# Performance work log

Measured on AMD Instinct MI355X. Metric: run time of the kernel, lower is better.

## Reference

```python
import jax, jax.numpy as jnp
import numpy as np

B, N, D = 32, 2048, 768
DEPTH, HEADS, GRID, NC = 12, 12, 10, 40
T = GRID * GRID + 1          # 100 pillars + cls token
HD = D // HEADS
SCALE = HD ** -0.5
INTERVAL = 0.2
MLP_H = 4 * D
EPS = 1e-5


def setup_inputs() -> dict:
    key = jax.random.key(0)
    ks = list(jax.random.split(key, 12))
    n = lambda k, s, std: (jax.random.normal(k, s, dtype=jnp.float32) * std)
    return {
        "x": jax.random.uniform(ks[0], (B, N, 3), minval=-1.0, maxval=1.0, dtype=jnp.float32),
        "W1": n(ks[1], (6, 32), 0.1),
        "W2": n(ks[2], (32, 64), 0.1),
        "W3": n(ks[3], (64, 128), 0.1),
        "Wa": n(ks[4], (256, D), 0.05),
        "bn_g": jnp.ones((GRID * GRID,), jnp.float32),
        "bn_b": jnp.zeros((GRID * GRID,), jnp.float32),
        "bn_mean": jnp.zeros((GRID * GRID,), jnp.float32),
        "bn_var": jnp.ones((GRID * GRID,), jnp.float32),
        "cls_token": jnp.zeros((1, 1, D), jnp.float32),
        "pos_embed": n(ks[5], (1, T, D), 0.02),
        "ln1_g": jnp.ones((DEPTH, D), jnp.float32), "ln1_b": jnp.zeros((DEPTH, D), jnp.float32),
        "qkv_w": n(ks[6], (DEPTH, D, 3 * D), 0.01),
        "proj_w": n(ks[7], (DEPTH, D, D), 0.01), "proj_b": jnp.zeros((DEPTH, D), jnp.float32),
        "ln2_g": jnp.ones((DEPTH, D), jnp.float32), "ln2_b": jnp.zeros((DEPTH, D), jnp.float32),
        "fc1_w": n(ks[8], (DEPTH, D, MLP_H), 0.01), "fc1_b": jnp.zeros((DEPTH, MLP_H), jnp.float32),
        "fc2_w": n(ks[9], (DEPTH, MLP_H, D), 0.01), "fc2_b": jnp.zeros((DEPTH, D), jnp.float32),
        "norm_g": jnp.ones((D,), jnp.float32), "norm_b": jnp.zeros((D,), jnp.float32),
        "head_w": n(ks[10], (D, NC), 0.01), "head_b": jnp.zeros((NC,), jnp.float32),
    }


def _layer_norm(x, g, b):
    m = jnp.mean(x, -1, keepdims=True)
    v = jnp.mean(jnp.square(x - m), -1, keepdims=True)
    return (x - m) * jax.lax.rsqrt(v + EPS) * g + b


def reference(x, W1, W2, W3, Wa, bn_g, bn_b, bn_mean, bn_var, cls_token, pos_embed,
              ln1_g, ln1_b, qkv_w, proj_w, proj_b, ln2_g, ln2_b,
              fc1_w, fc1_b, fc2_w, fc2_b, norm_g, norm_b, head_w, head_b):
    # ---- Pillar encoder (voxel bucketing via segment ops) ----
    # torch code reorders columns (y,z,x)->(z,y,x); voxel index uses (y,x)
    p = x[..., jnp.array([1, 0, 2])]                     # [B,N,3] = (z,y,x)
    yx = jnp.clip(p[..., 1:] + 1.0, 0.0, 1.99)
    idx = jnp.floor(yx / INTERVAL).astype(jnp.int32)     # [B,N,2] in [0,GRID)
    cell = (idx[..., 0] * GRID + idx[..., 1]
            + jnp.arange(B, dtype=jnp.int32)[:, None] * GRID * GRID).reshape(-1)
    pf = p.reshape(-1, 3)                                # [B*N,3]
    S = B * GRID * GRID
    cnt = jax.ops.segment_sum(jnp.ones((B * N,), pf.dtype), cell, num_segments=S)
    centroid = jax.ops.segment_sum(pf, cell, num_segments=S) / jnp.maximum(cnt, 1.0)[:, None]
    aug = jnp.concatenate([pf, pf - centroid[cell]], -1)  # [B*N,6]
    h = jax.nn.relu(aug @ W1)
    h = jax.nn.relu(h @ W2)
    h = jax.nn.relu(h @ W3)                               # [B*N,128]
    pooled = jax.ops.segment_max(h, cell, num_segments=S)  # per-pillar max
    h2 = jax.nn.relu(jnp.concatenate([h, pooled[cell]], -1) @ Wa)  # [B*N,768]
    pillar = jax.ops.segment_max(h2, cell, num_segments=S)
    pillar = jnp.where(cnt[:, None] > 0, pillar, 0.0)     # empty cells stay zero
    seq = pillar.reshape(B, GRID * GRID, D)               # flatten order = y*GRID+x
    # BatchNorm1d(100) over the sequence-position channel (eval mode)
    inv = bn_g * jax.lax.rsqrt(bn_var + EPS)
    seq = (seq - bn_mean[None, :, None]) * inv[None, :, None] + bn_b[None, :, None]

    # ---- ViT stack ----
    tokens = jnp.concatenate([jnp.broadcast_to(cls_token, (B, 1, D)), seq], 1) + pos_embed

    def block(hh, prm):
        g1, b1, qw, pw, pb, g2, b2, f1w, f1b, f2w, f2b = prm
        y = _layer_norm(hh, g1, b1)
        qkv = (y @ qw).reshape(B, T, 3, HEADS, HD)
        q, k, v = qkv[:, :, 0], qkv[:, :, 1], qkv[:, :, 2]   # [B,T,H,hd]
        attn = jax.nn.softmax(jnp.einsum('bqhd,bkhd->bhqk', q, k) * SCALE, -1)
        o = jnp.einsum('bhqk,bkhd->bqhd', attn, v).reshape(B, T, D)
        hh = hh + o @ pw + pb
        y = _layer_norm(hh, g2, b2)
        y = jax.nn.gelu(y @ f1w + f1b, approximate=False)
        hh = hh + y @ f2w + f2b
        return hh, None

    prms = (ln1_g, ln1_b, qkv_w, proj_w, proj_b, ln2_g, ln2_b, fc1_w, fc1_b, fc2_w, fc2_b)
    tokens, _ = jax.lax.scan(block, tokens, prms)
    out = _layer_norm(tokens, norm_g, norm_b)[:, 0] @ head_w + head_b  # cls head
    return out
```

## Files before the change

kernel.cpp:

```cpp
#include <hip/hip_runtime.h>

typedef __bf16 bf8 __attribute__((ext_vector_type(8)));
typedef float  f4  __attribute__((ext_vector_type(4)));
typedef unsigned long long uptr;

__device__ __forceinline__ void gload16(const void* g, void* l){
  __builtin_amdgcn_global_load_lds(
      (const __attribute__((address_space(1))) unsigned int*)(uptr)g,
      (__attribute__((address_space(3))) unsigned int*)(uptr)l,
      16, 0, 0);
}

__device__ __forceinline__ int xcd_chunk(int d, int nwg){
  int q = nwg >> 3, r = nwg & 7;
  int c = d & 7, j = d >> 3;
  return c*q + (c < r ? c : r) + j;
}


__global__ __launch_bounds__(256) void k_cell(const float* __restrict__ x, int* __restrict__ cellArr,
                                              float* __restrict__ cnt, float* __restrict__ cent){
  int p = blockIdx.x*256 + threadIdx.x;
  float x0 = x[p*3+0], x1 = x[p*3+1], x2 = x[p*3+2];
  float y0 = fminf(fmaxf(x0 + 1.0f, 0.0f), 1.99f);
  float y1 = fminf(fmaxf(x2 + 1.0f, 0.0f), 1.99f);
  int i0 = (int)floorf(y0 / 0.2f);
  int i1 = (int)floorf(y1 / 0.2f);
  int b = p >> 11;
  int cell = b*100 + i0*10 + i1;
  cellArr[p] = cell;
  atomicAdd(&cnt[cell], 1.0f);
  atomicAdd(&cent[cell*3+0], x1);
  atomicAdd(&cent[cell*3+1], x0);
  atomicAdd(&cent[cell*3+2], x2);
}

__global__ __launch_bounds__(256) void k_scan(const float* __restrict__ cnt,
                                              int* __restrict__ base, int* __restrict__ wptr){
  __shared__ int a[256];
  int tid = threadIdx.x;
  int start = tid*13, end = start+13; if (end > 3200) end = 3200;
  int local = 0;
  for (int i = start; i < end; i++) local += (int)cnt[i];
  a[tid] = local;
  __syncthreads();
  for (int off = 1; off < 256; off <<= 1){
    int t = (tid >= off) ? a[tid - off] : 0;
    __syncthreads();
    a[tid] += t;
    __syncthreads();
  }
  int run = a[tid] - local;
  for (int i = start; i < end; i++){
    base[i] = run; wptr[i] = run;
    run += (int)cnt[i];
  }
}

__global__ __launch_bounds__(256) void k_scatter(const int* __restrict__ cellArr,
                                                 int* __restrict__ wptr, int* __restrict__ order){
  int p = blockIdx.x*256 + threadIdx.x;
  int c = cellArr[p];
  int pos = atomicAdd(&wptr[c], 1);
  order[pos] = p;
}

__global__ __launch_bounds__(256) void k_pointmlp(const float* __restrict__ x,
    const float* __restrict__ W1, const float* __restrict__ W2, const float* __restrict__ W3,
    const float* __restrict__ cent, const float* __restrict__ cnt, const int* __restrict__ cellArr,
    const int* __restrict__ order, int* __restrict__ cellSlot, __bf16* __restrict__ A2){
  __shared__ float w1s[6*32];
  __shared__ float w2s[32*64];
  __shared__ float w3s[64*128];
  int tid = threadIdx.x;
  for (int i = tid; i < 192;  i += 256) w1s[i] = W1[i];
  for (int i = tid; i < 2048; i += 256) w2s[i] = W2[i];
  for (int i = tid; i < 8192; i += 256) w3s[i] = W3[i];
  __syncthreads();
  int s = blockIdx.x*256 + tid;
  int p = order[s];
  int cell = cellArr[p];
  cellSlot[s] = cell;
  float pf0 = x[p*3+1], pf1 = x[p*3+0], pf2 = x[p*3+2];
  float cc = fmaxf(cnt[cell], 1.0f);
  float a[6] = {pf0, pf1, pf2,
                pf0 - cent[cell*3+0]/cc, pf1 - cent[cell*3+1]/cc, pf2 - cent[cell*3+2]/cc};
  float h1[32];
  #pragma unroll
  for (int f = 0; f < 32; f++){
    float t = 0.f;
    #pragma unroll
    for (int i = 0; i < 6; i++) t += a[i]*w1s[i*32+f];
    h1[f] = fmaxf(t, 0.f);
  }
  float h2[64];
  #pragma unroll
  for (int f = 0; f < 64; f++){
    float t = 0.f;
    #pragma unroll
    for (int i = 0; i < 32; i++) t += h1[i]*w2s[i*64+f];
    h2[f] = fmaxf(t, 0.f);
  }
  for (int f0 = 0; f0 < 128; f0 += 8){
    __bf16 tmp[8];
    #pragma unroll
    for (int j = 0; j < 8; j++){
      float t = 0.f;
      #pragma unroll
      for (int i = 0; i < 64; i++) t += h2[i]*w3s[i*128+f0+j];
      tmp[j] = (__bf16)fmaxf(t, 0.f);
    }
    *reinterpret_cast<uint4*>(&A2[(size_t)s*256 + f0]) = *reinterpret_cast<uint4*>(tmp);
  }
}

__global__ __launch_bounds__(128) void k_poolh(const __bf16* __restrict__ A2,
    const int* __restrict__ base, const float* __restrict__ cnt, float* __restrict__ pooled){
  int c = blockIdx.x, f = threadIdx.x;
  int b0 = base[c], n = (int)cnt[c];
  float v = 0.f;
  for (int k = 0; k < n; k++) v = fmaxf(v, (float)A2[(size_t)(b0+k)*256 + f]);
  pooled[c*128 + f] = v;
}

__global__ __launch_bounds__(256) void k_fill(const float* __restrict__ pooled,
    const int* __restrict__ cellSlot, __bf16* __restrict__ A2){
  int idx = blockIdx.x*256 + threadIdx.x;
  int s = idx >> 4, f0 = (idx & 15) << 3;
  int cell = cellSlot[s];
  const float* pp = &pooled[cell*128 + f0];
  __bf16 tmp[8];
  #pragma unroll
  for (int j = 0; j < 8; j++) tmp[j] = (__bf16)pp[j];
  *reinterpret_cast<uint4*>(&A2[(size_t)s*256 + 128 + f0]) = *reinterpret_cast<uint4*>(tmp);
}

__global__ __launch_bounds__(256) void k_pillarpool(const __bf16* __restrict__ h2c,
    const int* __restrict__ base, const float* __restrict__ cnt, float* __restrict__ pillar){
  int c = blockIdx.x, tid = threadIdx.x;
  int b0 = base[c], n = (int)cnt[c];
  if (n == 0) return;
  for (int f = tid; f < 768; f += 256){
    float v = 0.f;
    for (int s = b0; s < b0 + n; s++) v = fmaxf(v, (float)h2c[(size_t)s*768 + f]);
    pillar[(size_t)c*768 + f] = v;
  }
}

__global__ void k_assemble(const float* __restrict__ pillar,
    const float* __restrict__ bn_g, const float* __restrict__ bn_b,
    const float* __restrict__ bn_mean, const float* __restrict__ bn_var,
    const float* __restrict__ cls_t, const float* __restrict__ pos,
    float* __restrict__ tokens){
  int idx = blockIdx.x*256 + threadIdx.x;
  int m = idx / 768, d = idx % 768;
  int b = m / 101, t = m % 101;
  float v;
  if (t == 0) v = cls_t[d];
  else {
    int s = t - 1;
    float pv = pillar[((size_t)b*100 + s)*768 + d];
    float inv = bn_g[s]*rsqrtf(bn_var[s] + 1e-5f);
    v = (pv - bn_mean[s])*inv + bn_b[s];
  }
  tokens[idx] = v + pos[t*768 + d];
}

__global__ __launch_bounds__(256) void k_transpose_all(
    const float* __restrict__ qw, const float* __restrict__ pw,
    const float* __restrict__ f1, const float* __restrict__ f2,
    const float* __restrict__ wa,
    __bf16* __restrict__ wq, __bf16* __restrict__ wp,
    __bf16* __restrict__ w1, __bf16* __restrict__ w2,
    __bf16* __restrict__ wwa){
  int id = blockIdx.x;
  size_t l = blockIdx.y;
  const float* W; __bf16* Wt; int K, N, kx, nx;
  if (id >= 1728){
    if (l != 0) return;
    id -= 1728; W=wa; Wt=wwa; K=256; N=768; kx=id%2; nx=id/2;
  }
  else if (id < 432){          W=qw+l*768*2304; Wt=wq+l*768*2304; K=768;  N=2304; kx=id%6;  nx=id/6; }
  else if (id < 576){ id-=432; W=pw+l*768*768;  Wt=wp+l*768*768;  K=768;  N=768;  kx=id%6;  nx=id/6; }
  else if (id < 1152){ id-=576;  W=f1+l*768*3072; Wt=w1+l*768*3072; K=768;  N=3072; kx=id%6;  nx=id/6; }
  else {               id-=1152; W=f2+l*3072*768; Wt=w2+l*3072*768; K=3072; N=768;  kx=id%24; nx=id/24; }
  __shared__ __bf16 t[32*136];
  int k0 = kx*128, n0 = nx*32;
  int tid = threadIdx.x;
  int kr = tid >> 3, nc = (tid & 7)*4;
  #pragma unroll
  for (int i = 0; i < 4; i++){
    int k = kr + i*32;
    float4 v = *reinterpret_cast<const float4*>(&W[(size_t)(k0+k)*N + n0 + nc]);
    float vv[4] = {v.x, v.y, v.z, v.w};
    #pragma unroll
    for (int jj = 0; jj < 4; jj++){
      int n = nc + jj;
      int slot = (k >> 3) ^ ((n >> 1) & 7);
      t[n*136 + slot*8 + (k & 7)] = (__bf16)vv[jj];
    }
  }
  __syncthreads();
  int nr = tid >> 4, sl = tid & 15;
  #pragma unroll
  for (int j = 0; j < 2; j++){
    int n = j*16 + nr;
    int slot = sl ^ ((n >> 1) & 7);
    *reinterpret_cast<uint4*>(&Wt[(size_t)(n0+n)*K + k0 + sl*8]) =
        *reinterpret_cast<uint4*>(&t[n*136 + slot*8]);
  }
}


__global__ __launch_bounds__(256) void k_gemm(const __bf16* __restrict__ A, const __bf16* __restrict__ Bt,
    const float* __restrict__ bias, const float* __restrict__ res,
    float* __restrict__ outF, __bf16* __restrict__ outB,
    int M, int N, int K, int act, int splitK){
  __shared__ alignas(16) __bf16 As[128*64];
  __shared__ alignas(16) __bf16 Bs[128*64];
  int tid  = threadIdx.x;
  int gx = gridDim.x, gy = gridDim.y;
  int d = blockIdx.y*gx + blockIdx.x;
  int w = xcd_chunk(d, gx*gy);
  int nx = w / gy, my = w % gy;
  int m0 = my*128, n0 = nx*128;
  int z = blockIdx.z;
  int kLen = K / splitK, k0 = z*kLen;
  int wave = tid >> 6, lane = tid & 63;
  int wm = (wave >> 1)*64, wn = (wave & 1)*64;
  int r16 = lane & 15, q = lane >> 4;
  int srow = tid >> 3;
  int sslot = tid & 7;
  int slotX[2];
  #pragma unroll
  for (int kk = 0; kk < 2; kk++) slotX[kk] = ((kk*4 + q) ^ (r16 & 7)) * 8;
  f4 acc[4][4];
  #pragma unroll
  for (int i = 0; i < 4; i++)
    #pragma unroll
    for (int j = 0; j < 4; j++) acc[i][j] = (f4){0.f,0.f,0.f,0.f};

  for (int kt = k0; kt < k0 + kLen; kt += 64){
    #pragma unroll
    for (int rr = 0; rr < 4; rr++){
      int row = rr*32 + srow;
      int scol = kt + ((sslot ^ (row & 7)) * 8);
      int gm = m0 + row; if (gm >= M) gm = M - 1;
      gload16(A  + (size_t)gm*K + scol, (char*)As + rr*4096 + tid*16);
      int gn = n0 + row;
      gload16(Bt + (size_t)gn*K + scol, (char*)Bs + rr*4096 + tid*16);
    }
    __syncthreads();
    #pragma unroll
    for (int kk = 0; kk < 2; kk++){
      bf8 af[4], bq[4];
      #pragma unroll
      for (int i = 0; i < 4; i++) af[i] = *reinterpret_cast<const bf8*>(&As[(wm + i*16 + r16)*64 + slotX[kk]]);
      #pragma unroll
      for (int j = 0; j < 4; j++) bq[j] = *reinterpret_cast<const bf8*>(&Bs[(wn + j*16 + r16)*64 + slotX[kk]]);
      #pragma unroll
      for (int i = 0; i < 4; i++)
        #pragma unroll
        for (int j = 0; j < 4; j++)
          acc[i][j] = __builtin_amdgcn_mfma_f32_16x16x32_bf16(af[i], bq[j], acc[i][j], 0, 0, 0);
    }
    __syncthreads();
  }

  #pragma unroll
  for (int i = 0; i < 4; i++){
    #pragma unroll
    for (int j = 0; j < 4; j++){
      int nn = n0 + wn + j*16 + r16;
      float bv = (bias && z == 0) ? bias[nn] : 0.f;
      #pragma unroll
      for (int r = 0; r < 4; r++){
        int m = m0 + wm + i*16 + q*4 + r;
        if (m >= M) continue;
        float v = acc[i][j][r] + bv;
        if (splitK > 1){
          atomicAdd(&outF[(size_t)m*N + nn], v);
        } else {
          if (act == 1) v = fmaxf(v, 0.f);
          else if (act == 2) v = 0.5f*v*(1.f + erff(v*0.70710678118654752f));
          if (outB){
            outB[(size_t)m*N + nn] = (__bf16)v;
          } else {
            float rv = res ? res[(size_t)m*N + nn] : 0.f;
            outF[(size_t)m*N + nn] = rv + v;
          }
        }
      }
    }
  }
}


__global__ __launch_bounds__(256) void k_ln(const float* __restrict__ in, const float* __restrict__ g,
    const float* __restrict__ bta, __bf16* __restrict__ outB, float* __restrict__ outF, int rowMul){
  int orow = blockIdx.x;
  const float* xr = in + (size_t)orow*rowMul*768;
  int tid = threadIdx.x;
  float v0 = xr[tid], v1 = xr[tid+256], v2 = xr[tid+512];
  float s = v0+v1+v2, s2 = v0*v0 + v1*v1 + v2*v2;
  #pragma unroll
  for (int off = 32; off > 0; off >>= 1){ s += __shfl_xor(s, off); s2 += __shfl_xor(s2, off); }
  __shared__ float rs[4], rq[4];
  int w = tid >> 6;
  if ((tid & 63) == 0){ rs[w] = s; rq[w] = s2; }
  __syncthreads();
  s = rs[0]+rs[1]+rs[2]+rs[3]; s2 = rq[0]+rq[1]+rq[2]+rq[3];
  float mean = s*(1.f/768.f);
  float var  = s2*(1.f/768.f) - mean*mean;
  float rstd = rsqrtf(var + 1e-5f);
  size_t ob = (size_t)orow*768;
  float y0 = (v0-mean)*rstd*g[tid]     + bta[tid];
  float y1 = (v1-mean)*rstd*g[tid+256] + bta[tid+256];
  float y2 = (v2-mean)*rstd*g[tid+512] + bta[tid+512];
  if (outB){ outB[ob+tid]=(__bf16)y0; outB[ob+tid+256]=(__bf16)y1; outB[ob+tid+512]=(__bf16)y2; }
  else     { outF[ob+tid]=y0;         outF[ob+tid+256]=y1;         outF[ob+tid+512]=y2; }
}


#define PSS 136
#define VTS 136

__global__ __launch_bounds__(256, 3) void k_attn(const __bf16* __restrict__ qkvB, __bf16* __restrict__ o){
  __shared__ alignas(16) __bf16 smem[64*VTS + 64*PSS];
  __bf16* Vt = smem;
  __bf16* Ps = smem + 64*VTS;
  int w = xcd_chunk(blockIdx.x, gridDim.x);
  int bh = w >> 1, half = w & 1;
  int b = bh / 12, h = bh % 12;
  int tid = threadIdx.x;
  const __bf16* basep = qkvB + (size_t)(b*101)*2304 + h*64;

  #pragma unroll
  for (int it = 0; it < 4; it++){
    int c = tid + it*256;
    int t = c >> 3, d0 = c & 7;
    bf8 v;
    if (t < 101){
      v = *reinterpret_cast<const bf8*>(&basep[(size_t)t*2304 + 1536 + d0*8]);
    } else {
      #pragma unroll
      for (int j = 0; j < 8; j++) v[j] = (__bf16)0.f;
    }
    #pragma unroll
    for (int j = 0; j < 8; j++){
      int jj = (j + d0) & 7;
      Vt[(d0*8 + jj)*VTS + t] = v[jj];
    }
  }

  int wave = tid >> 6, lane = tid & 63;
  int r16 = lane & 15, q = lane >> 4;
  int m0 = half*64 + wave*16;

  f4 sacc[7];
  #pragma unroll
  for (int j = 0; j < 7; j++) sacc[j] = (f4){0.f,0.f,0.f,0.f};
  #pragma unroll
  for (int kt = 0; kt < 64; kt += 32){
    int row = m0 + r16; if (row > 100) row = 100;
    bf8 aq = *reinterpret_cast<const bf8*>(&basep[(size_t)row*2304 + kt + q*8]);
    #pragma unroll
    for (int j = 0; j < 7; j++){
      int krow = j*16 + r16; if (krow > 100) krow = 100;
      bf8 kf = *reinterpret_cast<const bf8*>(&basep[(size_t)krow*2304 + 768 + kt + q*8]);
      sacc[j] = __builtin_amdgcn_mfma_f32_16x16x32_bf16(aq, kf, sacc[j], 0, 0, 0);
    }
  }

  #pragma unroll
  for (int r = 0; r < 4; r++){
    float s[7];
    #pragma unroll
    for (int j = 0; j < 7; j++){
      s[j] = sacc[j][r] * 0.125f;
      if (j == 6 && r16 >= 5) s[j] = -1e30f;
    }
    float mx = s[0];
    #pragma unroll
    for (int j = 1; j < 7; j++) mx = fmaxf(mx, s[j]);
    #pragma unroll
    for (int off2 = 1; off2 < 16; off2 <<= 1) mx = fmaxf(mx, __shfl_xor(mx, off2));
    float p[7], sum = 0.f;
    #pragma unroll
    for (int j = 0; j < 7; j++){ p[j] = __expf(s[j] - mx); sum += p[j]; }
    #pragma unroll
    for (int off2 = 1; off2 < 16; off2 <<= 1) sum += __shfl_xor(sum, off2);
    float inv = 1.f / sum;
    int lr = wave*16 + q*4 + r;
    #pragma unroll
    for (int j = 0; j < 7; j++) Ps[lr*PSS + j*16 + r16] = (__bf16)(p[j]*inv);
    Ps[lr*PSS + 112 + r16] = (__bf16)0.f;
  }
  __syncthreads();

  f4 oacc[4];
  #pragma unroll
  for (int n = 0; n < 4; n++) oacc[n] = (f4){0.f,0.f,0.f,0.f};
  #pragma unroll
  for (int kt = 0; kt < 128; kt += 32){
    bf8 af = *reinterpret_cast<const bf8*>(&Ps[(wave*16 + r16)*PSS + kt + q*8]);
    #pragma unroll
    for (int n = 0; n < 4; n++){
      bf8 bq = *reinterpret_cast<const bf8*>(&Vt[(n*16 + r16)*VTS + kt + q*8]);
      oacc[n] = __builtin_amdgcn_mfma_f32_16x16x32_bf16(af, bq, oacc[n], 0, 0, 0);
    }
  }

  #pragma unroll
  for (int n = 0; n < 4; n++){
    #pragma unroll
    for (int r = 0; r < 4; r++){
      int t = m0 + q*4 + r;
      if (t < 101)
        o[((size_t)(b*101 + t))*768 + h*64 + n*16 + r16] = (__bf16)oacc[n][r];
    }
  }
}

__global__ __launch_bounds__(256) void k_head(const float* __restrict__ cls, const float* __restrict__ hw,
                       const float* __restrict__ hb, float* __restrict__ out){
  int b = blockIdx.x;
  int tid = threadIdx.x;
  int c = tid % 40, s = tid / 40;
  __shared__ float part[6][40];
  if (s < 6){
    float acc = 0.f;
    for (int k = s*128; k < s*128 + 128; k++) acc += cls[b*768 + k]*hw[k*40 + c];
    part[s][c] = acc;
  }
  __syncthreads();
  if (tid < 40){
    float v = hb[tid];
    #pragma unroll
    for (int i = 0; i < 6; i++) v += part[i][tid];
    out[b*40 + tid] = v;
  }
}


extern "C" void kernel_launch(void* const* d_in, const int* in_sizes, int n_in,
                              void* d_out, int out_size, void* d_ws, size_t ws_size,
                              hipStream_t stream){
  const float* x       = (const float*)d_in[0];
  const float* W1      = (const float*)d_in[1];
  const float* W2      = (const float*)d_in[2];
  const float* W3      = (const float*)d_in[3];
  const float* Wa      = (const float*)d_in[4];
  const float* bn_g    = (const float*)d_in[5];
  const float* bn_b    = (const float*)d_in[6];
  const float* bn_mean = (const float*)d_in[7];
  const float* bn_var  = (const float*)d_in[8];
  const float* cls_t   = (const float*)d_in[9];
  const float* pos     = (const float*)d_in[10];
  const float* ln1_g   = (const float*)d_in[11];
  const float* ln1_b   = (const float*)d_in[12];
  const float* qkv_w   = (const float*)d_in[13];
  const float* proj_w  = (const float*)d_in[14];
  const float* proj_b  = (const float*)d_in[15];
  const float* ln2_g   = (const float*)d_in[16];
  const float* ln2_b   = (const float*)d_in[17];
  const float* fc1_w   = (const float*)d_in[18];
  const float* fc1_b   = (const float*)d_in[19];
  const float* fc2_w   = (const float*)d_in[20];
  const float* fc2_b   = (const float*)d_in[21];
  const float* norm_g  = (const float*)d_in[22];
  const float* norm_b  = (const float*)d_in[23];
  const float* head_w  = (const float*)d_in[24];
  const float* head_b  = (const float*)d_in[25];

  char* ws = (char*)d_ws;
  size_t off = 0;
  auto alloc = [&](size_t bytes)->void*{ void* p = ws + off; off += (bytes + 255) & ~(size_t)255; return p; };
  float* cnt     = (float*)alloc(3200*4);
  float* cent    = (float*)alloc(3200*3*4);
  float* pillar  = (float*)alloc((size_t)3200*768*4);
  size_t zbytes  = (size_t)((char*)pillar - (char*)cnt) + (size_t)3200*768*4;
  int*   base    = (int*)  alloc(3200*4);
  int*   wptr    = (int*)  alloc(3200*4);
  int*   order   = (int*)  alloc((size_t)65536*4);
  int*   cellSlot= (int*)  alloc((size_t)65536*4);
  int*   cellArr = (int*)  alloc((size_t)65536*4);
  float* pooled  = (float*)alloc((size_t)3200*128*4);
  float* tokens  = (float*)alloc((size_t)3232*768*4);
  float* cls     = (float*)alloc((size_t)32*768*4);
  __bf16* wWa    = (__bf16*)alloc((size_t)768*256*2);
  __bf16* wq12   = (__bf16*)alloc((size_t)12*768*2304*2);
  __bf16* wp12   = (__bf16*)alloc((size_t)12*768*768*2);
  __bf16* w112   = (__bf16*)alloc((size_t)12*768*3072*2);
  __bf16* w212   = (__bf16*)alloc((size_t)12*3072*768*2);
  size_t offR = off;
  __bf16* A2  = (__bf16*)alloc((size_t)65536*256*2);
  __bf16* h2c = (__bf16*)alloc((size_t)65536*768*2);
  size_t endPillarPhase = off;
  off = offR;
  __bf16* y    = (__bf16*)alloc((size_t)3232*768*2);
  __bf16* qkvB = (__bf16*)alloc((size_t)3232*2304*2);
  __bf16* o    = (__bf16*)alloc((size_t)3232*768*2);
  __bf16* mlp  = (__bf16*)alloc((size_t)3232*3072*2);
  if (off < endPillarPhase) off = endPillarPhase;
  (void)ws_size; (void)in_sizes; (void)n_in; (void)out_size;

  hipMemsetAsync(cnt, 0, zbytes, stream);

  k_transpose_all<<<dim3(1776,12),256,0,stream>>>(qkv_w, proj_w, fc1_w, fc2_w, Wa,
                                                  wq12, wp12, w112, w212, wWa);

  k_cell<<<256,256,0,stream>>>(x, cellArr, cnt, cent);
  k_scan<<<1,256,0,stream>>>(cnt, base, wptr);
  k_scatter<<<256,256,0,stream>>>(cellArr, wptr, order);
  k_pointmlp<<<256,256,0,stream>>>(x, W1, W2, W3, cent, cnt, cellArr, order, cellSlot, A2);
  k_poolh<<<3200,128,0,stream>>>(A2, base, cnt, pooled);
  k_fill<<<4096,256,0,stream>>>(pooled, cellSlot, A2);
  k_gemm<<<dim3(6,512),256,0,stream>>>(A2, wWa, nullptr, nullptr, nullptr, h2c, 65536, 768, 256, 1, 1);
  k_pillarpool<<<3200,256,0,stream>>>(h2c, base, cnt, pillar);
  k_assemble<<<9696,256,0,stream>>>(pillar, bn_g, bn_b, bn_mean, bn_var, cls_t, pos, tokens);

  for (int l = 0; l < 12; l++){
    __bf16* wq = wq12 + (size_t)l*768*2304;
    __bf16* wp = wp12 + (size_t)l*768*768;
    __bf16* w1 = w112 + (size_t)l*768*3072;
    __bf16* w2 = w212 + (size_t)l*3072*768;
    k_ln<<<3232,256,0,stream>>>(tokens, ln1_g + l*768, ln1_b + l*768, y, nullptr, 1);
    k_gemm<<<dim3(18,26),256,0,stream>>>(y, wq, nullptr, nullptr, nullptr, qkvB, 3232, 2304, 768, 0, 1);
    k_attn<<<768,256,0,stream>>>(qkvB, o);
    k_gemm<<<dim3(6,26,4),256,0,stream>>>(o, wp, proj_b + l*768, nullptr, tokens, nullptr,
                                          3232, 768, 768, 0, 4);
    k_ln<<<3232,256,0,stream>>>(tokens, ln2_g + l*768, ln2_b + l*768, y, nullptr, 1);
    k_gemm<<<dim3(24,26),256,0,stream>>>(y, w1, fc1_b + l*3072, nullptr, nullptr, mlp, 3232, 3072, 768, 2, 1);
    k_gemm<<<dim3(6,26,4),256,0,stream>>>(mlp, w2, fc2_b + l*768, nullptr, tokens, nullptr,
                                          3232, 768, 3072, 0, 4);
  }

  k_ln<<<32,256,0,stream>>>(tokens, norm_g, norm_b, nullptr, cls, 101);
  k_head<<<32,256,0,stream>>>(cls, head_w, head_b, (float*)d_out);
}
```

Before: 2.830 ms.

## Fuse pillar max-pool into Wa GEMM, vectorize LN and assemble, halve split-K

The Wa GEMM now max-reduces its ReLU outputs straight into the per-cell pillar buffer with integer atomicMax. This removes the 65536x768 bf16 intermediate and the separate pillar pool kernel. LayerNorm now processes one row per wave with float4 loads and no shared-memory reduction, and the token assembly kernel is vectorized with float4. Split-K for the proj and fc2 GEMMs drops from 4 to 2, cutting atomic traffic but giving fewer workgroups. The atomicMax-on-int trick relies on nonnegative values and a zeroed buffer, and it adds atomic contention on the pillar rows.

```diff
diff --git a/kernel.cpp b/kernel.cpp
--- a/kernel.cpp
+++ b/kernel.cpp
@@ -135,35 +135,30 @@
   *reinterpret_cast<uint4*>(&A2[(size_t)s*256 + 128 + f0]) = *reinterpret_cast<uint4*>(tmp);
 }
 
-__global__ __launch_bounds__(256) void k_pillarpool(const __bf16* __restrict__ h2c,
-    const int* __restrict__ base, const float* __restrict__ cnt, float* __restrict__ pillar){
-  int c = blockIdx.x, tid = threadIdx.x;
-  int b0 = base[c], n = (int)cnt[c];
-  if (n == 0) return;
-  for (int f = tid; f < 768; f += 256){
-    float v = 0.f;
-    for (int s = b0; s < b0 + n; s++) v = fmaxf(v, (float)h2c[(size_t)s*768 + f]);
-    pillar[(size_t)c*768 + f] = v;
-  }
-}
-
-__global__ void k_assemble(const float* __restrict__ pillar,
+__global__ __launch_bounds__(256) void k_assemble(const float* __restrict__ pillar,
     const float* __restrict__ bn_g, const float* __restrict__ bn_b,
     const float* __restrict__ bn_mean, const float* __restrict__ bn_var,
     const float* __restrict__ cls_t, const float* __restrict__ pos,
     float* __restrict__ tokens){
   int idx = blockIdx.x*256 + threadIdx.x;
-  int m = idx / 768, d = idx % 768;
+  int m = idx / 192, d4 = (idx % 192)*4;
   int b = m / 101, t = m % 101;
-  float v;
-  if (t == 0) v = cls_t[d];
-  else {
+  float4 pv = *reinterpret_cast<const float4*>(&pos[t*768 + d4]);
+  float4 out;
+  if (t == 0){
+    float4 ct = *reinterpret_cast<const float4*>(&cls_t[d4]);
+    out.x = ct.x + pv.x; out.y = ct.y + pv.y; out.z = ct.z + pv.z; out.w = ct.w + pv.w;
+  } else {
     int s = t - 1;
-    float pv = pillar[((size_t)b*100 + s)*768 + d];
+    float4 p = *reinterpret_cast<const float4*>(&pillar[((size_t)b*100 + s)*768 + d4]);
     float inv = bn_g[s]*rsqrtf(bn_var[s] + 1e-5f);
-    v = (pv - bn_mean[s])*inv + bn_b[s];
-  }
-  tokens[idx] = v + pos[t*768 + d];
+    float mu = bn_mean[s], bb = bn_b[s];
+    out.x = (p.x - mu)*inv + bb + pv.x;
+    out.y = (p.y - mu)*inv + bb + pv.y;
+    out.z = (p.z - mu)*inv + bb + pv.z;
+    out.w = (p.w - mu)*inv + bb + pv.w;
+  }
+  *reinterpret_cast<float4*>(&tokens[(size_t)m*768 + d4]) = out;
 }
 
 __global__ __launch_bounds__(256) void k_transpose_all(
@@ -215,7 +210,7 @@
 __global__ __launch_bounds__(256) void k_gemm(const __bf16* __restrict__ A, const __bf16* __restrict__ Bt,
     const float* __restrict__ bias, const float* __restrict__ res,
     float* __restrict__ outF, __bf16* __restrict__ outB,
-    int M, int N, int K, int act, int splitK){
+    int M, int N, int K, int act, int splitK, const int* __restrict__ cellSlot){
   __shared__ alignas(16) __bf16 As[128*64];
   __shared__ alignas(16) __bf16 Bs[128*64];
   int tid  = threadIdx.x;
@@ -280,6 +275,8 @@
         float v = acc[i][j][r] + bv;
         if (splitK > 1){
           atomicAdd(&outF[(size_t)m*N + nn], v);
+        } else if (act == 3){
+          atomicMax((int*)&outF[(size_t)cellSlot[m]*768 + nn], __float_as_int(fmaxf(v, 0.f)));
         } else {
           if (act == 1) v = fmaxf(v, 0.f);
           else if (act == 2) v = 0.5f*v*(1.f + erff(v*0.70710678118654752f));
@@ -298,27 +295,45 @@
 
 __global__ __launch_bounds__(256) void k_ln(const float* __restrict__ in, const float* __restrict__ g,
     const float* __restrict__ bta, __bf16* __restrict__ outB, float* __restrict__ outF, int rowMul){
-  int orow = blockIdx.x;
-  const float* xr = in + (size_t)orow*rowMul*768;
-  int tid = threadIdx.x;
-  float v0 = xr[tid], v1 = xr[tid+256], v2 = xr[tid+512];
-  float s = v0+v1+v2, s2 = v0*v0 + v1*v1 + v2*v2;
+  int row  = blockIdx.x*4 + (threadIdx.x >> 6);
+  int lane = threadIdx.x & 63;
+  int i0 = lane*4;
+  const float* xr = in + (size_t)row*rowMul*768;
+  float4 a = *reinterpret_cast<const float4*>(&xr[i0]);
+  float4 b = *reinterpret_cast<const float4*>(&xr[i0+256]);
+  float4 c = *reinterpret_cast<const float4*>(&xr[i0+512]);
+  float v[12] = {a.x,a.y,a.z,a.w, b.x,b.y,b.z,b.w, c.x,c.y,c.z,c.w};
+  float s = 0.f, s2 = 0.f;
+  #pragma unroll
+  for (int j = 0; j < 12; j++){ s += v[j]; s2 += v[j]*v[j]; }
   #pragma unroll
   for (int off = 32; off > 0; off >>= 1){ s += __shfl_xor(s, off); s2 += __shfl_xor(s2, off); }
-  __shared__ float rs[4], rq[4];
-  int w = tid >> 6;
-  if ((tid & 63) == 0){ rs[w] = s; rq[w] = s2; }
-  __syncthreads();
-  s = rs[0]+rs[1]+rs[2]+rs[3]; s2 = rq[0]+rq[1]+rq[2]+rq[3];
   float mean = s*(1.f/768.f);
-  float var  = s2*(1.f/768.f) - mean*mean;
-  float rstd = rsqrtf(var + 1e-5f);
-  size_t ob = (size_t)orow*768;
-  float y0 = (v0-mean)*rstd*g[tid]     + bta[tid];
-  float y1 = (v1-mean)*rstd*g[tid+256] + bta[tid+256];
-  float y2 = (v2-mean)*rstd*g[tid+512] + bta[tid+512];
-  if (outB){ outB[ob+tid]=(__bf16)y0; outB[ob+tid+256]=(__bf16)y1; outB[ob+tid+512]=(__bf16)y2; }
-  else     { outF[ob+tid]=y0;         outF[ob+tid+256]=y1;         outF[ob+tid+512]=y2; }
+  float rstd = rsqrtf(s2*(1.f/768.f) - mean*mean + 1e-5f);
+  float4 ga = *reinterpret_cast<const float4*>(&g[i0]);
+  float4 gb = *reinterpret_cast<const float4*>(&g[i0+256]);
+  float4 gc = *reinterpret_cast<const float4*>(&g[i0+512]);
+  float4 ba = *reinterpret_cast<const float4*>(&bta[i0]);
+  float4 bb = *reinterpret_cast<const float4*>(&bta[i0+256]);
+  float4 bc = *reinterpret_cast<const float4*>(&bta[i0+512]);
+  float gg[12] = {ga.x,ga.y,ga.z,ga.w, gb.x,gb.y,gb.z,gb.w, gc.x,gc.y,gc.z,gc.w};
+  float bv[12] = {ba.x,ba.y,ba.z,ba.w, bb.x,bb.y,bb.z,bb.w, bc.x,bc.y,bc.z,bc.w};
+  float y[12];
+  #pragma unroll
+  for (int j = 0; j < 12; j++) y[j] = (v[j]-mean)*rstd*gg[j] + bv[j];
+  size_t ob = (size_t)row*768;
+  if (outB){
+    __bf16 t[12];
+    #pragma unroll
+    for (int j = 0; j < 12; j++) t[j] = (__bf16)y[j];
+    *reinterpret_cast<uint2*>(&outB[ob+i0])     = *reinterpret_cast<uint2*>(&t[0]);
+    *reinterpret_cast<uint2*>(&outB[ob+i0+256]) = *reinterpret_cast<uint2*>(&t[4]);
+    *reinterpret_cast<uint2*>(&outB[ob+i0+512]) = *reinterpret_cast<uint2*>(&t[8]);
+  } else {
+    *reinterpret_cast<float4*>(&outF[ob+i0])     = (float4){y[0],y[1],y[2],y[3]};
+    *reinterpret_cast<float4*>(&outF[ob+i0+256]) = (float4){y[4],y[5],y[6],y[7]};
+    *reinterpret_cast<float4*>(&outF[ob+i0+512]) = (float4){y[8],y[9],y[10],y[11]};
+  }
 }
 
 
@@ -495,7 +510,6 @@
   __bf16* w212   = (__bf16*)alloc((size_t)12*3072*768*2);
   size_t offR = off;
   __bf16* A2  = (__bf16*)alloc((size_t)65536*256*2);
-  __bf16* h2c = (__bf16*)alloc((size_t)65536*768*2);
   size_t endPillarPhase = off;
   off = offR;
   __bf16* y    = (__bf16*)alloc((size_t)3232*768*2);
@@ -516,26 +530,28 @@
   k_pointmlp<<<256,256,0,stream>>>(x, W1, W2, W3, cent, cnt, cellArr, order, cellSlot, A2);
   k_poolh<<<3200,128,0,stream>>>(A2, base, cnt, pooled);
   k_fill<<<4096,256,0,stream>>>(pooled, cellSlot, A2);
-  k_gemm<<<dim3(6,512),256,0,stream>>>(A2, wWa, nullptr, nullptr, nullptr, h2c, 65536, 768, 256, 1, 1);
-  k_pillarpool<<<3200,256,0,stream>>>(h2c, base, cnt, pillar);
-  k_assemble<<<9696,256,0,stream>>>(pillar, bn_g, bn_b, bn_mean, bn_var, cls_t, pos, tokens);
+  k_gemm<<<dim3(6,512),256,0,stream>>>(A2, wWa, nullptr, nullptr, pillar, nullptr,
+                                       65536, 768, 256, 3, 1, cellSlot);
+  k_assemble<<<2424,256,0,stream>>>(pillar, bn_g, bn_b, bn_mean, bn_var, cls_t, pos, tokens);
 
   for (int l = 0; l < 12; l++){
     __bf16* wq = wq12 + (size_t)l*768*2304;
     __bf16* wp = wp12 + (size_t)l*768*768;
     __bf16* w1 = w112 + (size_t)l*768*3072;
     __bf16* w2 = w212 + (size_t)l*3072*768;
-    k_ln<<<3232,256,0,stream>>>(tokens, ln1_g + l*768, ln1_b + l*768, y, nullptr, 1);
-    k_gemm<<<dim3(18,26),256,0,stream>>>(y, wq, nullptr, nullptr, nullptr, qkvB, 3232, 2304, 768, 0, 1);
+    k_ln<<<808,256,0,stream>>>(tokens, ln1_g + l*768, ln1_b + l*768, y, nullptr, 1);
+    k_gemm<<<dim3(18,26),256,0,stream>>>(y, wq, nullptr, nullptr, nullptr, qkvB,
+                                         3232, 2304, 768, 0, 1, nullptr);
     k_attn<<<768,256,0,stream>>>(qkvB, o);
-    k_gemm<<<dim3(6,26,4),256,0,stream>>>(o, wp, proj_b + l*768, nullptr, tokens, nullptr,
-                                          3232, 768, 768, 0, 4);
-    k_ln<<<3232,256,0,stream>>>(tokens, ln2_g + l*768, ln2_b + l*768, y, nullptr, 1);
-    k_gemm<<<dim3(24,26),256,0,stream>>>(y, w1, fc1_b + l*3072, nullptr, nullptr, mlp, 3232, 3072, 768, 2, 1);
-    k_gemm<<<dim3(6,26,4),256,0,stream>>>(mlp, w2, fc2_b + l*768, nullptr, tokens, nullptr,
-                                          3232, 768, 3072, 0, 4);
-  }
-
-  k_ln<<<32,256,0,stream>>>(tokens, norm_g, norm_b, nullptr, cls, 101);
+    k_gemm<<<dim3(6,26,2),256,0,stream>>>(o, wp, proj_b + l*768, nullptr, tokens, nullptr,
+                                          3232, 768, 768, 0, 2, nullptr);
+    k_ln<<<808,256,0,stream>>>(tokens, ln2_g + l*768, ln2_b + l*768, y, nullptr, 1);
+    k_gemm<<<dim3(24,26),256,0,stream>>>(y, w1, fc1_b + l*3072, nullptr, nullptr, mlp,
+                                         3232, 3072, 768, 2, 1, nullptr);
+    k_gemm<<<dim3(6,26,2),256,0,stream>>>(mlp, w2, fc2_b + l*768, nullptr, tokens, nullptr,
+                                          3232, 768, 3072, 0, 2, nullptr);
+  }
+
+  k_ln<<<8,256,0,stream>>>(tokens, norm_g, norm_b, nullptr, cls, 101);
   k_head<<<32,256,0,stream>>>(cls, head_w, head_b, (float*)d_out);
 }
```

After: 3.117 ms. +10.1%, slower.
